# Optimization experiments

Measured on AMD Instinct MI355X. Metric: run time of the kernel, lower is better.

The kernel has to match this reference:

```python
import jax, jax.numpy as jnp
import numpy as np

N = 100000      # nodes
E = 1600000     # edges
IN = 128        # in_channels
HID = 32        # hidden_channels
HEADS = 4
G = 256         # number of graphs in the batch
NEG_SLOPE = 0.2


def setup_inputs() -> dict:
    key = jax.random.key(0)
    ks = jax.random.split(key, 20)
    s = 0.1
    d = {
        'x': jax.random.normal(ks[0], (N, IN), jnp.float32),
        'edge_index': jax.random.randint(ks[1], (2, E), 0, N, dtype=jnp.int64),
        'batch': jnp.sort(jax.random.randint(ks[2], (N,), 0, G, dtype=jnp.int64)),
        # conv1: IN -> HID per head, HEADS heads, concat
        'W1': jax.random.normal(ks[3], (IN, HEADS * HID), jnp.float32) * s,
        'a_src1': jax.random.normal(ks[4], (HEADS, HID), jnp.float32) * s,
        'a_dst1': jax.random.normal(ks[5], (HEADS, HID), jnp.float32) * s,
        'b1': jnp.zeros((HEADS * HID,), jnp.float32),
        # conv2: HEADS*HID -> HID per head, HEADS heads, concat
        'W2': jax.random.normal(ks[6], (HEADS * HID, HEADS * HID), jnp.float32) * s,
        'a_src2': jax.random.normal(ks[7], (HEADS, HID), jnp.float32) * s,
        'a_dst2': jax.random.normal(ks[8], (HEADS, HID), jnp.float32) * s,
        'b2': jnp.zeros((HEADS * HID,), jnp.float32),
        # conv3: HEADS*HID -> HID, 1 head, no concat (mean over heads is identity)
        'W3': jax.random.normal(ks[9], (HEADS * HID, HID), jnp.float32) * s,
        'a_src3': jax.random.normal(ks[10], (1, HID), jnp.float32) * s,
        'a_dst3': jax.random.normal(ks[11], (1, HID), jnp.float32) * s,
        'b3': jnp.zeros((HID,), jnp.float32),
        # final readout
        'fc_w': jax.random.normal(ks[12], (HID, 1), jnp.float32) * s,
        'fc_b': jnp.zeros((1,), jnp.float32),
    }
    return d


def _gat_layer(x, src, dst, W, a_s, a_d, b, concat):
    """One PyG-style GATConv: edge attention logits, per-destination softmax, scatter-aggregate."""
    n = x.shape[0]
    H, C = a_s.shape
    h = (x @ W).reshape(n, H, C)                       # [N, H, C]
    asrc = (h * a_s).sum(-1)                           # [N, H]
    adst = (h * a_d).sum(-1)                           # [N, H]
    e = jax.nn.leaky_relu(asrc[src] + adst[dst], NEG_SLOPE)   # [Etot, H]
    m = jax.ops.segment_max(e, dst, num_segments=n)    # per-dst max (self-loops guarantee non-empty)
    ex = jnp.exp(e - m[dst])
    den = jax.ops.segment_sum(ex, dst, num_segments=n)
    alpha = ex / (den[dst] + 1e-16)                    # segment softmax, [Etot, H]
    out = jax.ops.segment_sum(alpha[:, :, None] * h[src], dst, num_segments=n)  # [N, H, C]
    if concat:
        return out.reshape(n, H * C) + b
    return out.mean(axis=1) + b


def reference(x, edge_index, batch, W1, a_src1, a_dst1, b1, W2, a_src2, a_dst2, b2,
              W3, a_src3, a_dst3, b3, fc_w, fc_b):
    n = x.shape[0]
    loops = jnp.arange(n, dtype=edge_index.dtype)      # GATConv adds self-loops by default
    src = jnp.concatenate([edge_index[0], loops])
    dst = jnp.concatenate([edge_index[1], loops])

    h = jax.nn.elu(_gat_layer(x, src, dst, W1, a_src1, a_dst1, b1, True))
    h = jax.nn.elu(_gat_layer(h, src, dst, W2, a_src2, a_dst2, b2, True))
    h = jax.nn.elu(_gat_layer(h, src, dst, W3, a_src3, a_dst3, b3, False))

    counts = jax.ops.segment_sum(jnp.ones((n,), h.dtype), batch, num_segments=G)
    pooled = jax.ops.segment_sum(h, batch, num_segments=G) / jnp.maximum(counts, 1.0)[:, None]
    # dropout p=0.5 is identity in eval mode
    return pooled @ fc_w + fc_b                        # [G, 1]
```

## Files before the change

### kernel.cpp

```cpp
#include <hip/hip_runtime.h>
#include <hip/hip_bf16.h>
#include <math.h>

#define NEG_SLOPE 0.2f
#define CHUNK 6144

typedef short bf16x8 __attribute__((ext_vector_type(8)));
typedef float f32x4  __attribute__((ext_vector_type(4)));

__device__ __forceinline__ float leaky(float x){ return x > 0.f ? x : NEG_SLOPE*x; }
__device__ __forceinline__ float elu(float x){ return x > 0.f ? x : expm1f(x); }

__device__ __forceinline__ ushort f2bf(float f){
  uint u = __float_as_uint(f);
  u += 0x7fffu + ((u >> 16) & 1u);
  return (ushort)(u >> 16);
}
__device__ __forceinline__ uint pk2(float lo, float hi){
  return (uint)f2bf(lo) | ((uint)f2bf(hi) << 16);
}
__device__ __forceinline__ float2 bfpair(uint v){
  return make_float2(__uint_as_float(v << 16), __uint_as_float(v & 0xffff0000u));
}

__global__ __launch_bounds__(256) void k_histA(const int* __restrict__ ei, int E,
                                               int* __restrict__ bucketCount){
  __shared__ int hist[512];
  for (int b = threadIdx.x; b < 512; b += 256) hist[b] = 0;
  __syncthreads();
  int base = blockIdx.x * 2048;
  int cnt = min(2048, E - base);
  for (int i = threadIdx.x; i < cnt; i += 256)
    atomicAdd(&hist[ei[E + base + i] >> 8], 1);
  __syncthreads();
  for (int b = threadIdx.x; b < 512; b += 256)
    if (hist[b]) atomicAdd(&bucketCount[b], hist[b]);
}

__global__ __launch_bounds__(256) void k_scanB(const int* __restrict__ bucketCount, int NB,
                        int* __restrict__ bucketBase, int* __restrict__ gcursor, int E){
  __shared__ int s[512];
  for (int b = threadIdx.x; b < 512; b += 256)
    s[b] = (b < NB) ? bucketCount[b] : 0;
  __syncthreads();
  if (threadIdx.x == 0){
    int run = 0;
    for (int b = 0; b < NB; b++){ int v = s[b]; s[b] = run; run += v; }
  }
  __syncthreads();
  for (int b = threadIdx.x; b < NB; b += 256){
    bucketBase[b] = s[b]; gcursor[b] = s[b];
  }
  if (threadIdx.x == 0) bucketBase[NB] = E;
}

__global__ __launch_bounds__(256) void k_scatA(const int* __restrict__ ei, int E, int NB,
                         int* __restrict__ gcursor, uint* __restrict__ tmp){
  __shared__ uint stageS[CHUNK];
  __shared__ uint stageD[CHUNK];
  __shared__ int hist[512], pre[512], cur[512], gbase[512];
  __shared__ int scanArr[256];
  int tid = threadIdx.x;
  int base = blockIdx.x * CHUNK;
  int cnt = min(CHUNK, E - base);
  for (int b = tid; b < 512; b += 256) hist[b] = 0;
  __syncthreads();
  for (int i = tid; i < cnt; i += 256)
    atomicAdd(&hist[ei[E + base + i] >> 8], 1);
  __syncthreads();
  int a0 = hist[2*tid], a1 = hist[2*tid+1];
  scanArr[tid] = a0 + a1;
  __syncthreads();
  for (int st = 1; st < 256; st <<= 1){
    int v = (tid >= st) ? scanArr[tid - st] : 0;
    __syncthreads();
    scanArr[tid] += v;
    __syncthreads();
  }
  int eb = tid ? scanArr[tid-1] : 0;
  pre[2*tid] = eb;        cur[2*tid] = eb;
  pre[2*tid+1] = eb + a0; cur[2*tid+1] = eb + a0;
  if (2*tid < NB && a0 > 0)   gbase[2*tid]   = atomicAdd(&gcursor[2*tid],   a0);
  if (2*tid+1 < NB && a1 > 0) gbase[2*tid+1] = atomicAdd(&gcursor[2*tid+1], a1);
  __syncthreads();
  for (int i = tid; i < cnt; i += 256){
    int s = ei[base + i];
    int d = ei[E + base + i];
    int lpos = atomicAdd(&cur[d >> 8], 1);
    stageS[lpos] = (uint)s; stageD[lpos] = (uint)d;
  }
  __syncthreads();
  for (int i = tid; i < cnt; i += 256){
    uint d = stageD[i];
    int b = d >> 8;
    tmp[gbase[b] + (i - pre[b])] = (stageS[i] << 8) | (d & 255u);
  }
}

__global__ __launch_bounds__(256) void k_csr(const uint* __restrict__ tmp,
                      const int* __restrict__ bucketBase,
                      int N, int NB, int* __restrict__ offsets, int* __restrict__ csr){
  int b = blockIdx.x;
  int nodeBase = b << 8;
  int nNodes = min(256, N - nodeBase);
  int eBeg = bucketBase[b], eEnd = bucketBase[b+1];
  __shared__ int deg[256], cur[256];
  int tid = threadIdx.x;
  deg[tid] = 0;
  __syncthreads();
  for (int e = eBeg + tid; e < eEnd; e += 256)
    atomicAdd(&deg[tmp[e] & 255u], 1);
  __syncthreads();
  cur[tid] = deg[tid];
  __syncthreads();
  for (int st = 1; st < 256; st <<= 1){
    int w = (tid >= st) ? cur[tid - st] : 0;
    __syncthreads();
    cur[tid] += w;
    __syncthreads();
  }
  int excl = tid ? cur[tid-1] : 0;
  __syncthreads();
  cur[tid] = excl;
  if (tid < nNodes) offsets[nodeBase + tid] = eBeg + excl;
  if (b == NB-1 && tid == 0) offsets[N] = eEnd;
  __syncthreads();
  for (int e = eBeg + tid; e < eEnd; e += 256){
    uint u = tmp[e];
    int lpos = atomicAdd(&cur[u & 255u], 1);
    csr[eBeg + lpos] = (int)(u >> 8);
  }
}

template<int NT, int H>
__global__ __launch_bounds__(256) void k_wrepA(const float* __restrict__ W,
                    const float* __restrict__ a_s, const float* __restrict__ a_d,
                    ushort* __restrict__ Wf){
  constexpr int NTT = NT + 1;
  constexpr int M = NT*16;
  int idx = blockIdx.x*256 + threadIdx.x;
  if (idx >= NTT*4*64) return;
  int lane = idx & 63;
  int c = (idx >> 6) & 3;
  int t = idx >> 8;
  int j = lane & 15;
  int k0 = c*32 + (lane >> 4)*8;
  float vals[8];
  if (t < NT){
    int col = t*16 + j;
    const float* p0 = W + (size_t)k0*M + col;
    #pragma unroll
    for (int r = 0; r < 8; r++) vals[r] = p0[(size_t)r*M];
  } else {
    #pragma unroll
    for (int r = 0; r < 8; r++) vals[r] = 0.f;
    if (j < 2*H){
      int h = (j < H) ? j : (j - H);
      const float* av = (j < H) ? (a_s + h*32) : (a_d + h*32);
      #pragma unroll
      for (int r = 0; r < 8; r++){
        const float* wr = W + (size_t)(k0 + r)*M + h*32;
        float s = 0.f;
        for (int cc = 0; cc < 32; cc++) s += wr[cc]*av[cc];
        vals[r] = s;
      }
    }
  }
  uint4 o;
  o.x = pk2(vals[0], vals[1]); o.y = pk2(vals[2], vals[3]);
  o.z = pk2(vals[4], vals[5]); o.w = pk2(vals[6], vals[7]);
  *(uint4*)(Wf + (size_t)idx*8) = o;
}

template<int NT, bool A_F32, int H>
__global__ __launch_bounds__(256) void k_mgemm(const void* __restrict__ Xv,
                     const ushort* __restrict__ Wf, ushort* __restrict__ Y,
                     float* __restrict__ asrc, float* __restrict__ adst, int n){
  constexpr int NTT = NT + 1;
  constexpr int M = NT*16;
  int lane = threadIdx.x & 63;
  int l15 = lane & 15, q = lane >> 4;
  int wgid = blockIdx.x*4 + (threadIdx.x >> 6);
  int nchunks = (n + 15) >> 4;
  int stride = gridDim.x*4;

  bf16x8 bw[NTT][4];
  #pragma unroll
  for (int t = 0; t < NTT; t++)
    #pragma unroll
    for (int c = 0; c < 4; c++)
      bw[t][c] = *(const bf16x8*)(Wf + (size_t)(((t<<2)+c)*64 + lane)*8);

  int chunk = wgid;
  if (chunk >= nchunks) return;

  bf16x8 aCur[4], aNext[4];
  auto loadA = [&](int ck, bf16x8* a){
    int m = ck*16 + l15;
    if (m >= n) m = n - 1;
    if (A_F32){
      const float* X = (const float*)Xv + (size_t)m*128 + q*8;
      #pragma unroll
      for (int c = 0; c < 4; c++){
        float4 u0 = *(const float4*)(X + c*32);
        float4 u1 = *(const float4*)(X + c*32 + 4);
        uint4 pkd;
        pkd.x = pk2(u0.x, u0.y); pkd.y = pk2(u0.z, u0.w);
        pkd.z = pk2(u1.x, u1.y); pkd.w = pk2(u1.z, u1.w);
        union { uint4 u; bf16x8 v; } cv; cv.u = pkd;
        a[c] = cv.v;
      }
    } else {
      const ushort* X = (const ushort*)Xv + (size_t)m*128 + q*8;
      #pragma unroll
      for (int c = 0; c < 4; c++) a[c] = *(const bf16x8*)(X + c*32);
    }
  };

  loadA(chunk, aCur);
  while (true){
    int nx = chunk + stride;
    if (nx < nchunks) loadA(nx, aNext);
    f32x4 acc[NTT];
    #pragma unroll
    for (int t = 0; t < NTT; t++) acc[t] = (f32x4){0.f,0.f,0.f,0.f};
    #pragma unroll
    for (int c = 0; c < 4; c++)
      #pragma unroll
      for (int t = 0; t < NTT; t++)
        acc[t] = __builtin_amdgcn_mfma_f32_16x16x32_bf16(aCur[c], bw[t][c], acc[t], 0, 0, 0);
    int rowb = chunk*16 + q*4;
    #pragma unroll
    for (int t = 0; t < NT; t++)
      #pragma unroll
      for (int r = 0; r < 4; r++){
        int row = rowb + r;
        if (row < n) Y[(size_t)row*M + t*16 + l15] = f2bf(acc[t][r]);
      }
    #pragma unroll
    for (int r = 0; r < 4; r++){
      int row = rowb + r;
      if (row < n){
        float v = acc[NT][r];
        if (l15 < H)           asrc[(size_t)row*H + l15]       = v;
        else if (l15 < 2*H)    adst[(size_t)row*H + (l15 - H)] = v;
      }
    }
    if (nx >= nchunks) break;
    chunk = nx;
    #pragma unroll
    for (int c = 0; c < 4; c++) aCur[c] = aNext[c];
  }
}

template<bool OUT_BF16>
__global__ __launch_bounds__(256) void k_agg128f(const ushort* __restrict__ Hb,
                    const float* __restrict__ asrc, const float* __restrict__ adst,
                    const int* __restrict__ offsets, const int* __restrict__ csr_src,
                    const float* __restrict__ bias, void* __restrict__ Out, int n){
  __shared__ float lwAll[4][256];
  int wv = threadIdx.x >> 6;
  int lane = threadIdx.x & 63;
  float* lw = lwAll[wv];
  int node = blockIdx.x*4 + wv;
  if (node >= n) return;
  const int up = lane, ch = up*2, h0 = up >> 4;
  const uint* rows = (const uint*)Hb;
  int j0 = offsets[node], end = offsets[node+1];
  float4 adv = *(const float4*)(adst + (size_t)node*4);
  float adh = (h0==0)?adv.x:(h0==1)?adv.y:(h0==2)?adv.z:adv.w;
  float acc0 = 0.f, acc1 = 0.f, den = 0.f;
  {
    float w = __expf(leaky(asrc[(size_t)node*4 + h0] + adh));
    float2 f = bfpair(rows[(size_t)node*64 + up]);
    den += w; acc0 += w*f.x; acc1 += w*f.y;
  }
  for (int base = j0; base < end; base += 64){
    int m = min(64, end - base);
    int mR = (m + 7) & ~7;
    int sreg = node;
    if (lane < m){
      sreg = csr_src[base + lane];
      float4 a = *(const float4*)(asrc + (size_t)sreg*4);
      float4 w4;
      w4.x = __expf(leaky(a.x + adv.x));
      w4.y = __expf(leaky(a.y + adv.y));
      w4.z = __expf(leaky(a.z + adv.z));
      w4.w = __expf(leaky(a.w + adv.w));
      *(float4*)(lw + lane*4) = w4;
    } else if (lane < mR){
      *(float4*)(lw + lane*4) = make_float4(0.f, 0.f, 0.f, 0.f);
    }
    uint rA[8]; float wA[8];
    uint rB[8]; float wB[8];
    auto loadGroup = [&](int e, uint* r, float* w){
      #pragma unroll
      for (int k = 0; k < 8; k++){
        int s = __builtin_amdgcn_readlane(sreg, e + k);
        r[k] = rows[(size_t)(uint)s*64 + up];
      }
      #pragma unroll
      for (int k = 0; k < 8; k++) w[k] = lw[(e + k)*4 + h0];
    };
    auto consume = [&](const uint* r, const float* w){
      #pragma unroll
      for (int k = 0; k < 8; k++){
        float2 f = bfpair(r[k]);
        den += w[k]; acc0 += w[k]*f.x; acc1 += w[k]*f.y;
      }
    };
    loadGroup(0, rA, wA);
    int e = 8;
    for (; e + 16 <= mR; e += 16){
      loadGroup(e, rB, wB);
      consume(rA, wA);
      loadGroup(e + 8, rA, wA);
      consume(rB, wB);
    }
    if (e < mR){
      loadGroup(e, rB, wB);
      consume(rA, wA);
      consume(rB, wB);
    } else {
      consume(rA, wA);
    }
  }
  float inv = 1.f/(den + 1e-16f);
  float ox = elu(acc0*inv + bias[ch]);
  float oy = elu(acc1*inv + bias[ch+1]);
  if (OUT_BF16){
    ((uint*)Out)[(size_t)node*64 + up] = pk2(ox, oy);
  } else {
    *(float2*)((float*)Out + (size_t)node*128 + ch) = make_float2(ox, oy);
  }
}

__global__ __launch_bounds__(256) void k_agg32(const ushort* __restrict__ Hb,
                    const float* __restrict__ asrc, const float* __restrict__ adst,
                    const int* __restrict__ offsets, const int* __restrict__ csr_src,
                    const float* __restrict__ bias, float* __restrict__ Out, int n){
  __shared__ int   lsAll[4][4][16];
  __shared__ float lwAll[4][4][16];
  int wv = threadIdx.x >> 6;
  int lane = threadIdx.x & 63;
  int g = lane >> 4, i = lane & 15;
  int node = (blockIdx.x*4 + wv)*4 + g;
  if (node >= n) return;
  int* ls = lsAll[wv][g];
  float* lw = lwAll[wv][g];
  const uint* rows = (const uint*)Hb;
  float adn = adst[node];
  float acc0 = 0.f, acc1 = 0.f, den = 0.f;
  {
    float w = __expf(leaky(asrc[node] + adn));
    float2 f = bfpair(rows[(size_t)node*16 + i]);
    den += w; acc0 += w*f.x; acc1 += w*f.y;
  }
  int j0 = offsets[node], end = offsets[node+1];
  for (int base = j0; base < end; base += 16){
    int m = min(16, end - base);
    {
      int idx = base + i;
      bool v = idx < end;
      int s = v ? csr_src[idx] : node;
      ls[i] = s;
      lw[i] = v ? __expf(leaky(asrc[s] + adn)) : 0.f;
    }
    int mR = (m + 3) & ~3;
    for (int e = 0; e < mR; e += 4){
      int s0 = ls[e], s1 = ls[e+1], s2 = ls[e+2], s3 = ls[e+3];
      float w0 = lw[e], w1 = lw[e+1], w2 = lw[e+2], w3 = lw[e+3];
      uint r0 = rows[(size_t)s0*16 + i];
      uint r1 = rows[(size_t)s1*16 + i];
      uint r2 = rows[(size_t)s2*16 + i];
      uint r3 = rows[(size_t)s3*16 + i];
      float2 f0 = bfpair(r0), f1 = bfpair(r1), f2 = bfpair(r2), f3 = bfpair(r3);
      den  += (w0 + w1) + (w2 + w3);
      acc0 += w0*f0.x + w1*f1.x + w2*f2.x + w3*f3.x;
      acc1 += w0*f0.y + w1*f1.y + w2*f2.y + w3*f3.y;
    }
  }
  float inv = 1.f/(den + 1e-16f);
  int ch = i*2;
  float2 o;
  o.x = elu(acc0*inv + bias[ch]);
  o.y = elu(acc1*inv + bias[ch+1]);
  *(float2*)(Out + (size_t)node*32 + ch) = o;
}

__global__ __launch_bounds__(256) void k_bounds(const int* __restrict__ batch, int n, int G,
                                                int* __restrict__ gstart){
  int i = blockIdx.x*256 + threadIdx.x;
  if (i >= n) return;
  int b = batch[i];
  int bp = (i > 0) ? batch[i-1] : -1;
  for (int g = bp + 1; g <= b; g++) gstart[g] = i;
  if (i == n-1){
    for (int g = b + 1; g <= G; g++) gstart[g] = n;
  }
}

__global__ __launch_bounds__(256) void k_pool2(const float* __restrict__ H3,
                     const int* __restrict__ gstart, const float* __restrict__ fcw,
                     const float* __restrict__ fcb, float* __restrict__ out, int G){
  int g = blockIdx.x;
  int s0 = gstart[g], s1 = gstart[g+1];
  int tid = threadIdx.x;
  int c = tid & 31, r = tid >> 5;
  float sum = 0.f;
  for (int i = s0 + r; i < s1; i += 8)
    sum += H3[(size_t)i*32 + c];
  __shared__ float sh[8][32];
  sh[r][c] = sum;
  __syncthreads();
  if (tid < 32){
    float t = 0.f;
    #pragma unroll
    for (int k = 0; k < 8; k++) t += sh[k][tid];
    t *= fcw[tid];
    #pragma unroll
    for (int off = 16; off; off >>= 1) t += __shfl_down(t, off, 32);
    if (tid == 0){
      float cnt = (float)(s1 - s0); if (cnt < 1.f) cnt = 1.f;
      out[g] = t/cnt + fcb[0];
    }
  }
}

extern "C" void kernel_launch(void* const* d_in, const int* in_sizes, int n_in,
                              void* d_out, int out_size, void* d_ws, size_t ws_size,
                              hipStream_t stream){
  const float* x    = (const float*)d_in[0];
  const int*   ei   = (const int*)d_in[1];
  const int*   batch= (const int*)d_in[2];
  const float* W1   = (const float*)d_in[3];
  const float* as1  = (const float*)d_in[4];
  const float* ad1  = (const float*)d_in[5];
  const float* b1   = (const float*)d_in[6];
  const float* W2   = (const float*)d_in[7];
  const float* as2  = (const float*)d_in[8];
  const float* ad2  = (const float*)d_in[9];
  const float* b2   = (const float*)d_in[10];
  const float* W3   = (const float*)d_in[11];
  const float* as3  = (const float*)d_in[12];
  const float* ad3  = (const float*)d_in[13];
  const float* b3   = (const float*)d_in[14];
  const float* fcw  = (const float*)d_in[15];
  const float* fcb  = (const float*)d_in[16];
  float* out = (float*)d_out;

  const int N = in_sizes[0] / 128;
  const int E = in_sizes[1] / 2;
  const int G = out_size;
  const int NB = (N + 255) >> 8;

  char* p = (char*)d_ws;
  auto alloc = [&](size_t bytes) -> void* {
    void* r = (void*)p;
    p += (bytes + 255) & ~(size_t)255;
    return r;
  };
  ushort* bufH   = (ushort*)alloc((size_t)N*128*sizeof(ushort));
  ushort* aggB   = (ushort*)alloc((size_t)N*128*sizeof(ushort));
  float*  bufA32 = (float*)alloc((size_t)N*32*sizeof(float));
  float*  asrc   = (float*)alloc((size_t)N*4*sizeof(float));
  float*  adst   = (float*)alloc((size_t)N*4*sizeof(float));
  int*    offsets= (int*)alloc((size_t)(N+1)*sizeof(int));
  int*    csr    = (int*)alloc((size_t)E*sizeof(int));
  uint*   tmp    = (uint*)alloc((size_t)E*sizeof(uint));
  int*    bCount = (int*)alloc(512*sizeof(int));
  int*    bBase  = (int*)alloc(520*sizeof(int));
  int*    gcursor= (int*)alloc(512*sizeof(int));
  int*    gstart = (int*)alloc((size_t)(G+1)*sizeof(int));
  ushort* Wf1    = (ushort*)alloc(9*4*64*8*sizeof(ushort));
  ushort* Wf2    = (ushort*)alloc(9*4*64*8*sizeof(ushort));
  ushort* Wf3    = (ushort*)alloc(3*4*64*8*sizeof(ushort));

  hipMemsetAsync(bCount, 0, 512*sizeof(int), stream);

  k_wrepA<8,4><<<9, 256, 0, stream>>>(W1, as1, ad1, Wf1);
  k_wrepA<8,4><<<9, 256, 0, stream>>>(W2, as2, ad2, Wf2);
  k_wrepA<2,1><<<3, 256, 0, stream>>>(W3, as3, ad3, Wf3);

  k_histA<<<(E+2047)/2048, 256, 0, stream>>>(ei, E, bCount);
  k_scanB<<<1, 256, 0, stream>>>(bCount, NB, bBase, gcursor, E);
  k_scatA<<<(E+CHUNK-1)/CHUNK, 256, 0, stream>>>(ei, E, NB, gcursor, tmp);
  k_csr<<<NB, 256, 0, stream>>>(tmp, bBase, N, NB, offsets, csr);
  k_bounds<<<(N+255)/256, 256, 0, stream>>>(batch, N, G, gstart);

  const int GB = 512;
  const int NWB = (N + 3)/4;
  const int NWB32 = (N + 15)/16;
  k_mgemm<8, true , 4><<<GB, 256, 0, stream>>>(x, Wf1, bufH, asrc, adst, N);
  k_agg128f<true><<<NWB, 256, 0, stream>>>(bufH, asrc, adst, offsets, csr, b1, aggB, N);
  k_mgemm<8, false, 4><<<GB, 256, 0, stream>>>(aggB, Wf2, bufH, asrc, adst, N);
  k_agg128f<true><<<NWB, 256, 0, stream>>>(bufH, asrc, adst, offsets, csr, b2, aggB, N);
  k_mgemm<2, false, 1><<<GB, 256, 0, stream>>>(aggB, Wf3, bufH, asrc, adst, N);
  k_agg32<<<NWB32, 256, 0, stream>>>(bufH, asrc, adst, offsets, csr, b3, bufA32, N);
  k_pool2<<<G, 256, 0, stream>>>(bufA32, gstart, fcw, fcb, out, G);
}
```

Before: 448.5 us.

## Fuse GAT aggregation with next-layer GEMM and fuse layer-3 aggregation with pooling

The 128-wide aggregation kernel now also runs the next layer's projection. Each 1024-thread block aggregates 16 nodes into a bf16 row tile in shared memory, then MFMA waves multiply the tile by the next weight matrix and write both the features and the attention logits. This removes the intermediate aggregated-feature round trip to global memory and two GEMM launches. The final aggregation now dots each node with the FC weights and atomically accumulates into per-graph slots, striped 16 ways to spread contention, followed by a tiny finalize kernel. The cost is a block-wide sync with idle waves during the small GEMM phase, lower occupancy from the 1024-thread blocks, and float atomics that make the sum order nondeterministic.

After: 485.0 us. 1.08x slower.

```diff
diff --git a/kernel.cpp b/kernel.cpp
--- a/kernel.cpp
+++ b/kernel.cpp
@@ -253,92 +253,130 @@
   }
 }
 
-template<bool OUT_BF16>
-__global__ __launch_bounds__(256) void k_agg128f(const ushort* __restrict__ Hb,
+template<int NT, int HOUT>
+__global__ __launch_bounds__(1024) void k_aggGemm(const ushort* __restrict__ Hb,
                     const float* __restrict__ asrc, const float* __restrict__ adst,
                     const int* __restrict__ offsets, const int* __restrict__ csr_src,
-                    const float* __restrict__ bias, void* __restrict__ Out, int n){
-  __shared__ float lwAll[4][256];
+                    const float* __restrict__ biasAgg, const ushort* __restrict__ Wf,
+                    ushort* __restrict__ Y, float* __restrict__ asrcN,
+                    float* __restrict__ adstN, int n){
+  constexpr int NTT = NT + 1;
+  constexpr int M = NT*16;
+  __shared__ float lwAll[16][256];
+  __shared__ ushort rowBuf[16][136];
   int wv = threadIdx.x >> 6;
   int lane = threadIdx.x & 63;
-  float* lw = lwAll[wv];
-  int node = blockIdx.x*4 + wv;
-  if (node >= n) return;
+  int node = blockIdx.x*16 + wv;
   const int up = lane, ch = up*2, h0 = up >> 4;
   const uint* rows = (const uint*)Hb;
-  int j0 = offsets[node], end = offsets[node+1];
-  float4 adv = *(const float4*)(adst + (size_t)node*4);
-  float adh = (h0==0)?adv.x:(h0==1)?adv.y:(h0==2)?adv.z:adv.w;
-  float acc0 = 0.f, acc1 = 0.f, den = 0.f;
-  {
-    float w = __expf(leaky(asrc[(size_t)node*4 + h0] + adh));
-    float2 f = bfpair(rows[(size_t)node*64 + up]);
-    den += w; acc0 += w*f.x; acc1 += w*f.y;
-  }
-  for (int base = j0; base < end; base += 64){
-    int m = min(64, end - base);
-    int mR = (m + 7) & ~7;
-    int sreg = node;
-    if (lane < m){
-      sreg = csr_src[base + lane];
-      float4 a = *(const float4*)(asrc + (size_t)sreg*4);
-      float4 w4;
-      w4.x = __expf(leaky(a.x + adv.x));
-      w4.y = __expf(leaky(a.y + adv.y));
-      w4.z = __expf(leaky(a.z + adv.z));
-      w4.w = __expf(leaky(a.w + adv.w));
-      *(float4*)(lw + lane*4) = w4;
-    } else if (lane < mR){
-      *(float4*)(lw + lane*4) = make_float4(0.f, 0.f, 0.f, 0.f);
-    }
-    uint rA[8]; float wA[8];
-    uint rB[8]; float wB[8];
-    auto loadGroup = [&](int e, uint* r, float* w){
-      #pragma unroll
-      for (int k = 0; k < 8; k++){
-        int s = __builtin_amdgcn_readlane(sreg, e + k);
-        r[k] = rows[(size_t)(uint)s*64 + up];
-      }
-      #pragma unroll
-      for (int k = 0; k < 8; k++) w[k] = lw[(e + k)*4 + h0];
-    };
-    auto consume = [&](const uint* r, const float* w){
-      #pragma unroll
-      for (int k = 0; k < 8; k++){
-        float2 f = bfpair(r[k]);
-        den += w[k]; acc0 += w[k]*f.x; acc1 += w[k]*f.y;
-      }
-    };
-    loadGroup(0, rA, wA);
-    int e = 8;
-    for (; e + 16 <= mR; e += 16){
-      loadGroup(e, rB, wB);
-      consume(rA, wA);
-      loadGroup(e + 8, rA, wA);
-      consume(rB, wB);
-    }
-    if (e < mR){
-      loadGroup(e, rB, wB);
-      consume(rA, wA);
-      consume(rB, wB);
-    } else {
-      consume(rA, wA);
-    }
-  }
-  float inv = 1.f/(den + 1e-16f);
-  float ox = elu(acc0*inv + bias[ch]);
-  float oy = elu(acc1*inv + bias[ch+1]);
-  if (OUT_BF16){
-    ((uint*)Out)[(size_t)node*64 + up] = pk2(ox, oy);
+  float* lw = lwAll[wv];
+
+  if (node < n){
+    int j0 = offsets[node], end = offsets[node+1];
+    float4 adv = *(const float4*)(adst + (size_t)node*4);
+    float adh = (h0==0)?adv.x:(h0==1)?adv.y:(h0==2)?adv.z:adv.w;
+    float acc0 = 0.f, acc1 = 0.f, den = 0.f;
+    {
+      float w = __expf(leaky(asrc[(size_t)node*4 + h0] + adh));
+      float2 f = bfpair(rows[(size_t)node*64 + up]);
+      den += w; acc0 += w*f.x; acc1 += w*f.y;
+    }
+    for (int base = j0; base < end; base += 64){
+      int m = min(64, end - base);
+      int mR = (m + 7) & ~7;
+      int sreg = node;
+      if (lane < m){
+        sreg = csr_src[base + lane];
+        float4 a = *(const float4*)(asrc + (size_t)sreg*4);
+        float4 w4;
+        w4.x = __expf(leaky(a.x + adv.x));
+        w4.y = __expf(leaky(a.y + adv.y));
+        w4.z = __expf(leaky(a.z + adv.z));
+        w4.w = __expf(leaky(a.w + adv.w));
+        *(float4*)(lw + lane*4) = w4;
+      } else if (lane < mR){
+        *(float4*)(lw + lane*4) = make_float4(0.f, 0.f, 0.f, 0.f);
+      }
+      uint rA[8]; float wA[8];
+      uint rB[8]; float wB[8];
+      auto loadGroup = [&](int e, uint* r, float* w){
+        #pragma unroll
+        for (int k = 0; k < 8; k++){
+          int s = __builtin_amdgcn_readlane(sreg, e + k);
+          r[k] = rows[(size_t)(uint)s*64 + up];
+        }
+        #pragma unroll
+        for (int k = 0; k < 8; k++) w[k] = lw[(e + k)*4 + h0];
+      };
+      auto consume = [&](const uint* r, const float* w){
+        #pragma unroll
+        for (int k = 0; k < 8; k++){
+          float2 f = bfpair(r[k]);
+          den += w[k]; acc0 += w[k]*f.x; acc1 += w[k]*f.y;
+        }
+      };
+      loadGroup(0, rA, wA);
+      int e = 8;
+      for (; e + 16 <= mR; e += 16){
+        loadGroup(e, rB, wB);
+        consume(rA, wA);
+        loadGroup(e + 8, rA, wA);
+        consume(rB, wB);
+      }
+      if (e < mR){
+        loadGroup(e, rB, wB);
+        consume(rA, wA);
+        consume(rB, wB);
+      } else {
+        consume(rA, wA);
+      }
+    }
+    float inv = 1.f/(den + 1e-16f);
+    float ox = elu(acc0*inv + biasAgg[ch]);
+    float oy = elu(acc1*inv + biasAgg[ch+1]);
+    *(uint*)&rowBuf[wv][ch] = pk2(ox, oy);
   } else {
-    *(float2*)((float*)Out + (size_t)node*128 + ch) = make_float2(ox, oy);
-  }
-}
-
-__global__ __launch_bounds__(256) void k_agg32(const ushort* __restrict__ Hb,
+    *(uint*)&rowBuf[wv][ch] = 0u;
+  }
+  __syncthreads();
+  if (wv >= NTT) return;
+
+  int l15 = lane & 15, q = lane >> 4;
+  bf16x8 bw[4];
+  #pragma unroll
+  for (int c = 0; c < 4; c++)
+    bw[c] = *(const bf16x8*)(Wf + (size_t)(((wv<<2)+c)*64 + lane)*8);
+  f32x4 acc = (f32x4){0.f,0.f,0.f,0.f};
+  #pragma unroll
+  for (int c = 0; c < 4; c++){
+    bf16x8 a = *(const bf16x8*)&rowBuf[l15][c*32 + q*8];
+    acc = __builtin_amdgcn_mfma_f32_16x16x32_bf16(a, bw[c], acc, 0, 0, 0);
+  }
+  int rowb = blockIdx.x*16 + q*4;
+  if (wv < NT){
+    #pragma unroll
+    for (int r = 0; r < 4; r++){
+      int row = rowb + r;
+      if (row < n) Y[(size_t)row*M + wv*16 + l15] = f2bf(acc[r]);
+    }
+  } else {
+    #pragma unroll
+    for (int r = 0; r < 4; r++){
+      int row = rowb + r;
+      if (row < n){
+        float v = acc[r];
+        if (l15 < HOUT)          asrcN[(size_t)row*HOUT + l15]          = v;
+        else if (l15 < 2*HOUT)   adstN[(size_t)row*HOUT + (l15 - HOUT)] = v;
+      }
+    }
+  }
+}
+
+__global__ __launch_bounds__(256) void k_agg32pool(const ushort* __restrict__ Hb,
                     const float* __restrict__ asrc, const float* __restrict__ adst,
                     const int* __restrict__ offsets, const int* __restrict__ csr_src,
-                    const float* __restrict__ bias, float* __restrict__ Out, int n){
+                    const float* __restrict__ bias, const float* __restrict__ fcw,
+                    const int* __restrict__ batch, float* __restrict__ pool, int n){
   __shared__ int   lsAll[4][4][16];
   __shared__ float lwAll[4][4][16];
   int wv = threadIdx.x >> 6;
@@ -382,10 +420,11 @@
   }
   float inv = 1.f/(den + 1e-16f);
   int ch = i*2;
-  float2 o;
-  o.x = elu(acc0*inv + bias[ch]);
-  o.y = elu(acc1*inv + bias[ch+1]);
-  *(float2*)(Out + (size_t)node*32 + ch) = o;
+  float2 fw = *(const float2*)(fcw + ch);
+  float t = elu(acc0*inv + bias[ch])*fw.x + elu(acc1*inv + bias[ch+1])*fw.y;
+  #pragma unroll
+  for (int off = 1; off < 16; off <<= 1) t += __shfl_xor(t, off, 16);
+  if (i == 0) atomicAdd(&pool[(size_t)batch[node]*16 + (node & 15)], t);
 }
 
 __global__ __launch_bounds__(256) void k_bounds(const int* __restrict__ batch, int n, int G,
@@ -400,31 +439,17 @@
   }
 }
 
-__global__ __launch_bounds__(256) void k_pool2(const float* __restrict__ H3,
-                     const int* __restrict__ gstart, const float* __restrict__ fcw,
-                     const float* __restrict__ fcb, float* __restrict__ out, int G){
-  int g = blockIdx.x;
-  int s0 = gstart[g], s1 = gstart[g+1];
-  int tid = threadIdx.x;
-  int c = tid & 31, r = tid >> 5;
-  float sum = 0.f;
-  for (int i = s0 + r; i < s1; i += 8)
-    sum += H3[(size_t)i*32 + c];
-  __shared__ float sh[8][32];
-  sh[r][c] = sum;
-  __syncthreads();
-  if (tid < 32){
-    float t = 0.f;
-    #pragma unroll
-    for (int k = 0; k < 8; k++) t += sh[k][tid];
-    t *= fcw[tid];
-    #pragma unroll
-    for (int off = 16; off; off >>= 1) t += __shfl_down(t, off, 32);
-    if (tid == 0){
-      float cnt = (float)(s1 - s0); if (cnt < 1.f) cnt = 1.f;
-      out[g] = t/cnt + fcb[0];
-    }
-  }
+__global__ __launch_bounds__(256) void k_poolfin(const float* __restrict__ pool,
+                    const int* __restrict__ gstart, const float* __restrict__ fcb,
+                    float* __restrict__ out, int G){
+  int g = blockIdx.x*256 + threadIdx.x;
+  if (g >= G) return;
+  float s = 0.f;
+  #pragma unroll
+  for (int k = 0; k < 16; k++) s += pool[(size_t)g*16 + k];
+  float cnt = (float)(gstart[g+1] - gstart[g]);
+  if (cnt < 1.f) cnt = 1.f;
+  out[g] = s/cnt + fcb[0];
 }
 
 extern "C" void kernel_launch(void* const* d_in, const int* in_sizes, int n_in,
@@ -460,11 +485,13 @@
     p += (bytes + 255) & ~(size_t)255;
     return r;
   };
-  ushort* bufH   = (ushort*)alloc((size_t)N*128*sizeof(ushort));
-  ushort* aggB   = (ushort*)alloc((size_t)N*128*sizeof(ushort));
-  float*  bufA32 = (float*)alloc((size_t)N*32*sizeof(float));
-  float*  asrc   = (float*)alloc((size_t)N*4*sizeof(float));
-  float*  adst   = (float*)alloc((size_t)N*4*sizeof(float));
+  ushort* bufH1  = (ushort*)alloc((size_t)N*128*sizeof(ushort));
+  ushort* bufH2  = (ushort*)alloc((size_t)N*128*sizeof(ushort));
+  ushort* bufH3  = (ushort*)alloc((size_t)N*32*sizeof(ushort));
+  float*  asrcA  = (float*)alloc((size_t)N*4*sizeof(float));
+  float*  adstA  = (float*)alloc((size_t)N*4*sizeof(float));
+  float*  asrcB  = (float*)alloc((size_t)N*4*sizeof(float));
+  float*  adstB  = (float*)alloc((size_t)N*4*sizeof(float));
   int*    offsets= (int*)alloc((size_t)(N+1)*sizeof(int));
   int*    csr    = (int*)alloc((size_t)E*sizeof(int));
   uint*   tmp    = (uint*)alloc((size_t)E*sizeof(uint));
@@ -472,11 +499,13 @@
   int*    bBase  = (int*)alloc(520*sizeof(int));
   int*    gcursor= (int*)alloc(512*sizeof(int));
   int*    gstart = (int*)alloc((size_t)(G+1)*sizeof(int));
+  float*  pool   = (float*)alloc((size_t)G*16*sizeof(float));
   ushort* Wf1    = (ushort*)alloc(9*4*64*8*sizeof(ushort));
   ushort* Wf2    = (ushort*)alloc(9*4*64*8*sizeof(ushort));
   ushort* Wf3    = (ushort*)alloc(3*4*64*8*sizeof(ushort));
 
   hipMemsetAsync(bCount, 0, 512*sizeof(int), stream);
+  hipMemsetAsync(pool, 0, (size_t)G*16*sizeof(float), stream);
 
   k_wrepA<8,4><<<9, 256, 0, stream>>>(W1, as1, ad1, Wf1);
   k_wrepA<8,4><<<9, 256, 0, stream>>>(W2, as2, ad2, Wf2);
@@ -489,13 +518,14 @@
   k_bounds<<<(N+255)/256, 256, 0, stream>>>(batch, N, G, gstart);
 
   const int GB = 512;
-  const int NWB = (N + 3)/4;
+  const int NCB = (N + 15)/16;
   const int NWB32 = (N + 15)/16;
-  k_mgemm<8, true , 4><<<GB, 256, 0, stream>>>(x, Wf1, bufH, asrc, adst, N);
-  k_agg128f<true><<<NWB, 256, 0, stream>>>(bufH, asrc, adst, offsets, csr, b1, aggB, N);
-  k_mgemm<8, false, 4><<<GB, 256, 0, stream>>>(aggB, Wf2, bufH, asrc, adst, N);
-  k_agg128f<true><<<NWB, 256, 0, stream>>>(bufH, asrc, adst, offsets, csr, b2, aggB, N);
-  k_mgemm<2, false, 1><<<GB, 256, 0, stream>>>(aggB, Wf3, bufH, asrc, adst, N);
-  k_agg32<<<NWB32, 256, 0, stream>>>(bufH, asrc, adst, offsets, csr, b3, bufA32, N);
-  k_pool2<<<G, 256, 0, stream>>>(bufA32, gstart, fcw, fcb, out, G);
-}
+  k_mgemm<8, true, 4><<<GB, 256, 0, stream>>>(x, Wf1, bufH1, asrcA, adstA, N);
+  k_aggGemm<8, 4><<<NCB, 1024, 0, stream>>>(bufH1, asrcA, adstA, offsets, csr,
+                                            b1, Wf2, bufH2, asrcB, adstB, N);
+  k_aggGemm<2, 1><<<NCB, 1024, 0, stream>>>(bufH2, asrcB, adstB, offsets, csr,
+                                            b2, Wf3, bufH3, asrcA, adstA, N);
+  k_agg32pool<<<NWB32, 256, 0, stream>>>(bufH3, asrcA, adstA, offsets, csr,
+                                         b3, fcw, batch, pool, N);
+  k_poolfin<<<(G+255)/256, 256, 0, stream>>>(pool, gstart, fcb, out, G);
+}
```
